# Kernel optimization log

Measured on AMD Instinct MI355X. Metric: run time of the kernel, lower is better.

Reference implementation:

```python
import jax, jax.numpy as jnp
import numpy as np

N = 10000   # nodes
E = 320000  # edges
G = 64      # graphs in batch
D = 256     # gnn embedding dim
A = 118     # atomic_num_dim
OUT = 100   # spectrum dim
NUM_GINE = 2


def setup_inputs() -> dict:
    key = jax.random.key(0)
    ks = jax.random.split(key, 16)
    inp = {
        'atomic_num': jax.random.normal(ks[0], (N, A), dtype=jnp.float32),
        'length': jax.random.uniform(ks[1], (E,), dtype=jnp.float32),
        'src': jax.random.randint(ks[2], (E,), 0, N, dtype=jnp.int32),
        'dst': jax.random.randint(ks[3], (E,), 0, N, dtype=jnp.int32),
        'graph_ids': jnp.sort(jax.random.randint(ks[4], (N,), 0, G, dtype=jnp.int32)),
        # parameters
        'W_node': jax.random.normal(ks[5], (A, D), dtype=jnp.float32) / np.sqrt(A),
        'b_node': jnp.zeros((D,), dtype=jnp.float32),
        'W_edge': jax.random.normal(ks[6], (1, D), dtype=jnp.float32),
        'b_edge': jnp.zeros((D,), dtype=jnp.float32),
        'gine_eps': jnp.zeros((NUM_GINE,), dtype=jnp.float32),  # learnable eps per GINEConv
        'W_gnn': jax.random.normal(ks[7], (NUM_GINE, D, D), dtype=jnp.float32) / np.sqrt(D),
        'b_gnn': jnp.zeros((NUM_GINE, D), dtype=jnp.float32),
        'eps_param': jnp.array([1e-3], dtype=jnp.float32),  # unify_vector eps
        'W_mlp': jax.random.normal(ks[8], (D, OUT), dtype=jnp.float32) / np.sqrt(D),
        'b_mlp': jnp.zeros((OUT,), dtype=jnp.float32),
    }
    return inp


def reference(atomic_num, length, src, dst, graph_ids,
              W_node, b_node, W_edge, b_edge,
              gine_eps, W_gnn, b_gnn, eps_param, W_mlp, b_mlp):
    # node / edge embeddings
    h = atomic_num @ W_node + b_node            # [N, D]
    e = length[:, None] @ W_edge + b_edge       # [E, D]
    # GINEConv layers: m_ij = relu(h_src + e_ij); h_i' = W((1+eps)h_i + sum_j m_ij) + b
    for i in range(NUM_GINE):
        m = jax.nn.relu(h[src] + e)             # [E, D] gather + elementwise
        agg = jax.ops.segment_sum(m, dst, num_segments=N)  # scatter-sum to dst nodes
        h = ((1.0 + gine_eps[i]) * h + agg) @ W_gnn[i] + b_gnn[i]
    # sum_nodes pooling per graph
    feat = jax.ops.segment_sum(h, graph_ids, num_segments=G)  # [G, D]
    # unify_vector: global min/max normalization
    mn = jnp.min(feat)
    mx = jnp.max(feat)
    feat = (feat - mn) / (eps_param[0] + mx - mn)
    # MLP head (no hidden layers): Linear(D, 100)
    return feat @ W_mlp + b_mlp                 # [G, 100]
```

## Files before the change

### kernel.cpp

```cpp
#include <hip/hip_runtime.h>
#include <hip/hip_bf16.h>

#define N_NODES 10000
#define N_EDGES 320000
#define N_GRAPHS 64
#define DIM 256
#define ADIM 118
#define OUTD 100
#define CAP 192

typedef short bf8_t __attribute__((ext_vector_type(8)));
typedef float f4_t  __attribute__((ext_vector_type(4)));

__device__ __forceinline__ unsigned short f2bf(float f) {
    unsigned u = __float_as_uint(f);
    u += 0x7FFFu + ((u >> 16) & 1u);
    return (unsigned short)(u >> 16);
}
__device__ __forceinline__ float bf2f(unsigned short s) {
    return __uint_as_float(((unsigned)s) << 16);
}

__global__ __launch_bounds__(256) void convW_k(
    const float* __restrict__ Wn, const float* __restrict__ Wg,
    unsigned short* __restrict__ WnT, unsigned short* __restrict__ WgT,
    int* __restrict__ cursor, float* __restrict__ feat) {
    int i = blockIdx.x * 256 + threadIdx.x;
    if (i < 32768) {
        int c = i >> 7, k = i & 127;
        WnT[i] = (k < ADIM) ? f2bf(Wn[k * DIM + c]) : (unsigned short)0;
    } else {
        int j = i - 32768;
        int l = j >> 16, rem = j & 65535;
        int c = rem >> 8, k = rem & 255;
        WgT[j] = f2bf(Wg[l * 65536 + k * DIM + c]);
    }
    if (i < N_NODES) cursor[i] = i * CAP;
    if (i < N_GRAPHS * DIM) feat[i] = 0.f;
}

__global__ __launch_bounds__(256) void fill_k(
    const int* __restrict__ src, const int* __restrict__ dst,
    const float* __restrict__ len, int* __restrict__ cursor,
    int2* __restrict__ epack) {
    int j = blockIdx.x * 256 + threadIdx.x;
    if (j >= N_EDGES) return;
    int d = dst[j];
    int pos = atomicAdd(&cursor[d], 1);
    if (pos < d * CAP + CAP)
        epack[pos] = make_int2(src[j], __float_as_int(len[j]));
}

#define AST 136
__global__ __launch_bounds__(256) void node_embed_k(
    const float* __restrict__ an, const unsigned short* __restrict__ WnT,
    const float* __restrict__ bn, unsigned short* __restrict__ hbf) {
    __shared__ unsigned short xs[16 * AST];
    const int base = blockIdx.x * 16;
    const int tid = threadIdx.x;
    for (int i = tid; i < 16 * (AST - ADIM); i += 256) {
        int r = i / (AST - ADIM);
        int c = i - r * (AST - ADIM);
        xs[r * AST + ADIM + c] = 0;
    }
    for (int i = tid; i < 16 * ADIM; i += 256) {
        int r = i / ADIM;
        int c = i - r * ADIM;
        xs[r * AST + c] = f2bf(an[(size_t)(base + r) * ADIM + c]);
    }
    __syncthreads();
    const int wave = tid >> 6, lane = tid & 63;
    const int m = lane & 15, quad = lane >> 4;
    bf8_t afrag[4];
    #pragma unroll
    for (int s = 0; s < 4; ++s)
        afrag[s] = *(const bf8_t*)&xs[m * AST + s * 32 + quad * 8];
    const int colbase = wave * 64;
    f4_t acc[4];
    #pragma unroll
    for (int ct = 0; ct < 4; ++ct) acc[ct] = (f4_t){0.f, 0.f, 0.f, 0.f};
    #pragma unroll
    for (int ct = 0; ct < 4; ++ct) {
        const unsigned short* wp = WnT + (size_t)(colbase + ct * 16 + m) * 128 + quad * 8;
        #pragma unroll
        for (int s = 0; s < 4; ++s) {
            bf8_t bfrag = *(const bf8_t*)(wp + s * 32);
            acc[ct] = __builtin_amdgcn_mfma_f32_16x16x32_bf16(afrag[s], bfrag, acc[ct], 0, 0, 0);
        }
    }
    #pragma unroll
    for (int ct = 0; ct < 4; ++ct) {
        int col = colbase + ct * 16 + m;
        float bb = bn[col];
        #pragma unroll
        for (int r = 0; r < 4; ++r)
            hbf[(size_t)(base + quad * 4 + r) * DIM + col] = f2bf(acc[ct][r] + bb);
    }
}

__global__ __launch_bounds__(256) void gather_k(
    const unsigned short* __restrict__ hbf, const int* __restrict__ cursor,
    const int2* __restrict__ epack, const float* __restrict__ We,
    const float* __restrict__ be, const float* __restrict__ epsp, int layer,
    unsigned short* __restrict__ xbf) {
    const int wave = threadIdx.x >> 6, lane = threadIdx.x & 63;
    const int node = __builtin_amdgcn_readfirstlane(blockIdx.x * 4 + wave);
    const int sub = lane >> 5;
    const int dp = (lane & 31) * 8;
    float4 wa = *(const float4*)(We + dp);
    float4 wc = *(const float4*)(We + dp + 4);
    float4 b0 = *(const float4*)(be + dp);
    float4 b1 = *(const float4*)(be + dp + 4);
    float w[8]  = {wa.x, wa.y, wa.z, wa.w, wc.x, wc.y, wc.z, wc.w};
    float bv[8] = {b0.x, b0.y, b0.z, b0.w, b1.x, b1.y, b1.z, b1.w};
    float acc[8];
    #pragma unroll
    for (int i = 0; i < 8; ++i) acc[i] = 0.f;
    const unsigned short* hb = hbf + dp;
    const int lo = node * CAP;
    const int cnt = min(__builtin_amdgcn_readfirstlane(cursor[node]) - lo, CAP);
    const int2* ep = epack + lo;
    int t = 0;
#define PAIR(pa, pb) { \
    int s = sub ? (pb).x : (pa).x; \
    float l = __int_as_float(sub ? (pb).y : (pa).y); \
    bf8_t a = *(const bf8_t*)(hb + (size_t)s * DIM); \
    _Pragma("unroll") \
    for (int d = 0; d < 8; ++d) \
        acc[d] += fmaxf(bf2f((unsigned short)a[d]) + fmaf(l, w[d], bv[d]), 0.f); }
    for (; t + 7 < cnt; t += 8) {
        int2 q0 = ep[t + 0], q1 = ep[t + 1], q2 = ep[t + 2], q3 = ep[t + 3];
        int2 q4 = ep[t + 4], q5 = ep[t + 5], q6 = ep[t + 6], q7 = ep[t + 7];
        PAIR(q0, q1) PAIR(q2, q3) PAIR(q4, q5) PAIR(q6, q7)
    }
    for (; t + 1 < cnt; t += 2) {
        int2 q0 = ep[t], q1 = ep[t + 1];
        PAIR(q0, q1)
    }
    if (t < cnt) {
        int2 q0 = ep[t];
        float l = __int_as_float(q0.y);
        bf8_t a = *(const bf8_t*)(hb + (size_t)q0.x * DIM);
        if (sub == 0) {
            #pragma unroll
            for (int d = 0; d < 8; ++d)
                acc[d] += fmaxf(bf2f((unsigned short)a[d]) + fmaf(l, w[d], bv[d]), 0.f);
        }
    }
#undef PAIR
    #pragma unroll
    for (int d = 0; d < 8; ++d)
        acc[d] += __shfl(acc[d], lane ^ 32, 64);
    if (sub == 0) {
        const float eps1 = 1.f + epsp[layer];
        bf8_t hv = *(const bf8_t*)(hbf + (size_t)node * DIM + dp);
        bf8_t o;
        #pragma unroll
        for (int d = 0; d < 8; ++d)
            o[d] = (short)f2bf(fmaf(eps1, bf2f((unsigned short)hv[d]), acc[d]));
        *(bf8_t*)(xbf + (size_t)node * DIM + dp) = o;
    }
}

#define XST 264
__global__ __launch_bounds__(256) void update_k(
    const unsigned short* __restrict__ xbf,
    const unsigned short* __restrict__ WT, const float* __restrict__ b,
    unsigned short* __restrict__ hout,
    const int* __restrict__ gid, float* __restrict__ feat, int do_pool) {
    __shared__ unsigned short xs[16 * XST];
    __shared__ int gids[16];
    const int rb = blockIdx.x >> 1;
    const int halfc = blockIdx.x & 1;
    const int base = rb * 16;
    const int tid = threadIdx.x;
    #pragma unroll
    for (int cch = tid; cch < 512; cch += 256) {
        int rr = cch >> 5, k0 = (cch & 31) * 8;
        *(bf8_t*)&xs[rr * XST + k0] = *(const bf8_t*)(xbf + (size_t)(base + rr) * DIM + k0);
    }
    if (do_pool && tid < 16) gids[tid] = gid[base + tid];
    __syncthreads();
    const int wave = tid >> 6, lane = tid & 63;
    const int m = lane & 15, quad = lane >> 4;
    bf8_t afrag[8];
    #pragma unroll
    for (int s = 0; s < 8; ++s)
        afrag[s] = *(const bf8_t*)&xs[m * XST + s * 32 + quad * 8];
    const int colbase = halfc * 128 + wave * 32;
    f4_t acc[2];
    #pragma unroll
    for (int ct = 0; ct < 2; ++ct) acc[ct] = (f4_t){0.f, 0.f, 0.f, 0.f};
    #pragma unroll
    for (int ct = 0; ct < 2; ++ct) {
        const unsigned short* wp = WT + (size_t)(colbase + ct * 16 + m) * DIM + quad * 8;
        #pragma unroll
        for (int s = 0; s < 8; ++s) {
            bf8_t bfrag = *(const bf8_t*)(wp + s * 32);
            acc[ct] = __builtin_amdgcn_mfma_f32_16x16x32_bf16(afrag[s], bfrag, acc[ct], 0, 0, 0);
        }
    }
    if (!do_pool) {
        #pragma unroll
        for (int ct = 0; ct < 2; ++ct) {
            int col = colbase + ct * 16 + m;
            float bb = b[col];
            #pragma unroll
            for (int r = 0; r < 4; ++r)
                hout[(size_t)(base + quad * 4 + r) * DIM + col] = f2bf(acc[ct][r] + bb);
        }
    } else {
        #pragma unroll
        for (int ct = 0; ct < 2; ++ct) {
            int col = colbase + ct * 16 + m;
            float bb = b[col];
            float run = 0.f;
            int cur = gids[quad * 4];
            #pragma unroll
            for (int r = 0; r < 4; ++r) {
                int g = gids[quad * 4 + r];
                if (g != cur) {
                    atomicAdd(&feat[(size_t)cur * DIM + col], run);
                    run = 0.f;
                    cur = g;
                }
                run += acc[ct][r] + bb;
            }
            atomicAdd(&feat[(size_t)cur * DIM + col], run);
        }
    }
}

__global__ __launch_bounds__(256) void headmm_k(
    const float* __restrict__ feat, const float* __restrict__ Wm,
    const float* __restrict__ bm, const float* __restrict__ epsp,
    float* __restrict__ out) {
    __shared__ float frow[DIM];
    __shared__ float smn[4], smx[4], sMn, sMx;
    const int g = blockIdx.x;
    const int tid = threadIdx.x;
    float mn = 3.4e38f, mx = -3.4e38f;
    for (int i = tid; i < N_GRAPHS * DIM; i += 256) {
        float v = feat[i];
        mn = fminf(mn, v);
        mx = fmaxf(mx, v);
    }
    frow[tid] = feat[g * DIM + tid];
    #pragma unroll
    for (int off = 32; off > 0; off >>= 1) {
        mn = fminf(mn, __shfl_down(mn, off, 64));
        mx = fmaxf(mx, __shfl_down(mx, off, 64));
    }
    const int wave = tid >> 6, lane = tid & 63;
    if (lane == 0) { smn[wave] = mn; smx[wave] = mx; }
    __syncthreads();
    if (tid == 0) {
        sMn = fminf(fminf(smn[0], smn[1]), fminf(smn[2], smn[3]));
        sMx = fmaxf(fmaxf(smx[0], smx[1]), fmaxf(smx[2], smx[3]));
    }
    __syncthreads();
    if (tid < OUTD) {
        const float mnv = sMn;
        const float inv = 1.f / (epsp[0] + sMx - mnv);
        float acc = 0.f;
        for (int d = 0; d < DIM; ++d)
            acc += (frow[d] - mnv) * Wm[d * OUTD + tid];
        out[g * OUTD + tid] = acc * inv + bm[tid];
    }
}

extern "C" void kernel_launch(void* const* d_in, const int* in_sizes, int n_in,
                              void* d_out, int out_size, void* d_ws, size_t ws_size,
                              hipStream_t stream) {
    const float* atomic_num = (const float*)d_in[0];
    const float* length     = (const float*)d_in[1];
    const int*   src        = (const int*)d_in[2];
    const int*   dst        = (const int*)d_in[3];
    const int*   gid        = (const int*)d_in[4];
    const float* W_node     = (const float*)d_in[5];
    const float* b_node     = (const float*)d_in[6];
    const float* W_edge     = (const float*)d_in[7];
    const float* b_edge     = (const float*)d_in[8];
    const float* gine_eps   = (const float*)d_in[9];
    const float* W_gnn      = (const float*)d_in[10];
    const float* b_gnn      = (const float*)d_in[11];
    const float* eps_param  = (const float*)d_in[12];
    const float* W_mlp      = (const float*)d_in[13];
    const float* b_mlp      = (const float*)d_in[14];
    float* out = (float*)d_out;

    float* feat = (float*)d_ws;
    int* cursor = (int*)(feat + (size_t)N_GRAPHS * DIM);
    int2* epack = (int2*)(cursor + N_NODES + 4);
    unsigned short* hbf0 = (unsigned short*)(epack + (size_t)N_NODES * CAP);
    unsigned short* hbf1 = hbf0 + (size_t)N_NODES * DIM;
    unsigned short* xbf  = hbf1 + (size_t)N_NODES * DIM;
    unsigned short* WnT  = xbf + (size_t)N_NODES * DIM;
    unsigned short* WgT  = WnT + 256 * 128;

    convW_k<<<640, 256, 0, stream>>>(W_node, W_gnn, WnT, WgT, cursor, feat);
    fill_k<<<N_EDGES / 256, 256, 0, stream>>>(src, dst, length, cursor, epack);
    node_embed_k<<<N_NODES / 16, 256, 0, stream>>>(atomic_num, WnT, b_node, hbf0);

    gather_k<<<N_NODES / 4, 256, 0, stream>>>(
        hbf0, cursor, epack, W_edge, b_edge, gine_eps, 0, xbf);
    update_k<<<(N_NODES / 16) * 2, 256, 0, stream>>>(
        xbf, WgT, b_gnn, hbf1, gid, feat, 0);
    gather_k<<<N_NODES / 4, 256, 0, stream>>>(
        hbf1, cursor, epack, W_edge, b_edge, gine_eps, 1, xbf);
    update_k<<<(N_NODES / 16) * 2, 256, 0, stream>>>(
        xbf, WgT + 256 * 256, b_gnn + DIM, hbf0, gid, feat, 1);

    headmm_k<<<N_GRAPHS, 256, 0, stream>>>(feat, W_mlp, b_mlp, eps_param, out);
}
```

Measured before the change: 217.8 us.

## Split gather across feature quarters with one scalar element per lane

Restructures the edge gather so that each wave covers one node and a 64-wide quarter of the feature dimension, with each lane loading a single bf16 element, instead of half-waves loading 8-element vectors across two edges. The grid grows fourfold and block indices are remapped so the four quarter-blocks of the same node group sit next to each other, which is meant to improve parallelism and keep loads coalesced. The output is written with a nontemporal store. In exchange, each edge index is now read four times and the row gathers become 2-byte scalar loads rather than 16-byte vector loads, which adds instruction and request overhead.

After: 228.5 us. 1.05x slower.

```diff
diff --git a/kernel.cpp b/kernel.cpp
--- a/kernel.cpp
+++ b/kernel.cpp
@@ -104,62 +104,49 @@
     const float* __restrict__ be, const float* __restrict__ epsp, int layer,
     unsigned short* __restrict__ xbf) {
     const int wave = threadIdx.x >> 6, lane = threadIdx.x & 63;
-    const int node = __builtin_amdgcn_readfirstlane(blockIdx.x * 4 + wave);
-    const int sub = lane >> 5;
-    const int dp = (lane & 31) * 8;
-    float4 wa = *(const float4*)(We + dp);
-    float4 wc = *(const float4*)(We + dp + 4);
-    float4 b0 = *(const float4*)(be + dp);
-    float4 b1 = *(const float4*)(be + dp + 4);
-    float w[8]  = {wa.x, wa.y, wa.z, wa.w, wc.x, wc.y, wc.z, wc.w};
-    float bv[8] = {b0.x, b0.y, b0.z, b0.w, b1.x, b1.y, b1.z, b1.w};
-    float acc[8];
-    #pragma unroll
-    for (int i = 0; i < 8; ++i) acc[i] = 0.f;
-    const unsigned short* hb = hbf + dp;
+    const int b = blockIdx.x;
+    const int quarter = b & 3;
+    const int node = __builtin_amdgcn_readfirstlane(
+        ((b >> 3) * 2 + ((b >> 2) & 1)) * 4 + wave);
+    const int d = quarter * 64 + lane;
+    const float w  = We[d];
+    const float bb = be[d];
+    const unsigned short* hb = hbf + d;
+    float acc = 0.f;
     const int lo = node * CAP;
     const int cnt = min(__builtin_amdgcn_readfirstlane(cursor[node]) - lo, CAP);
     const int2* ep = epack + lo;
     int t = 0;
-#define PAIR(pa, pb) { \
-    int s = sub ? (pb).x : (pa).x; \
-    float l = __int_as_float(sub ? (pb).y : (pa).y); \
-    bf8_t a = *(const bf8_t*)(hb + (size_t)s * DIM); \
-    _Pragma("unroll") \
-    for (int d = 0; d < 8; ++d) \
-        acc[d] += fmaxf(bf2f((unsigned short)a[d]) + fmaf(l, w[d], bv[d]), 0.f); }
     for (; t + 7 < cnt; t += 8) {
         int2 q0 = ep[t + 0], q1 = ep[t + 1], q2 = ep[t + 2], q3 = ep[t + 3];
         int2 q4 = ep[t + 4], q5 = ep[t + 5], q6 = ep[t + 6], q7 = ep[t + 7];
-        PAIR(q0, q1) PAIR(q2, q3) PAIR(q4, q5) PAIR(q6, q7)
-    }
-    for (; t + 1 < cnt; t += 2) {
-        int2 q0 = ep[t], q1 = ep[t + 1];
-        PAIR(q0, q1)
-    }
-    if (t < cnt) {
+        unsigned short a0 = hb[(size_t)q0.x * DIM];
+        unsigned short a1 = hb[(size_t)q1.x * DIM];
+        unsigned short a2 = hb[(size_t)q2.x * DIM];
+        unsigned short a3 = hb[(size_t)q3.x * DIM];
+        unsigned short a4 = hb[(size_t)q4.x * DIM];
+        unsigned short a5 = hb[(size_t)q5.x * DIM];
+        unsigned short a6 = hb[(size_t)q6.x * DIM];
+        unsigned short a7 = hb[(size_t)q7.x * DIM];
+        acc += fmaxf(bf2f(a0) + fmaf(__int_as_float(q0.y), w, bb), 0.f);
+        acc += fmaxf(bf2f(a1) + fmaf(__int_as_float(q1.y), w, bb), 0.f);
+        acc += fmaxf(bf2f(a2) + fmaf(__int_as_float(q2.y), w, bb), 0.f);
+        acc += fmaxf(bf2f(a3) + fmaf(__int_as_float(q3.y), w, bb), 0.f);
+        acc += fmaxf(bf2f(a4) + fmaf(__int_as_float(q4.y), w, bb), 0.f);
+        acc += fmaxf(bf2f(a5) + fmaf(__int_as_float(q5.y), w, bb), 0.f);
+        acc += fmaxf(bf2f(a6) + fmaf(__int_as_float(q6.y), w, bb), 0.f);
+        acc += fmaxf(bf2f(a7) + fmaf(__int_as_float(q7.y), w, bb), 0.f);
+    }
+    for (; t < cnt; ++t) {
         int2 q0 = ep[t];
-        float l = __int_as_float(q0.y);
-        bf8_t a = *(const bf8_t*)(hb + (size_t)q0.x * DIM);
-        if (sub == 0) {
-            #pragma unroll
-            for (int d = 0; d < 8; ++d)
-                acc[d] += fmaxf(bf2f((unsigned short)a[d]) + fmaf(l, w[d], bv[d]), 0.f);
-        }
-    }
-#undef PAIR
-    #pragma unroll
-    for (int d = 0; d < 8; ++d)
-        acc[d] += __shfl(acc[d], lane ^ 32, 64);
-    if (sub == 0) {
-        const float eps1 = 1.f + epsp[layer];
-        bf8_t hv = *(const bf8_t*)(hbf + (size_t)node * DIM + dp);
-        bf8_t o;
-        #pragma unroll
-        for (int d = 0; d < 8; ++d)
-            o[d] = (short)f2bf(fmaf(eps1, bf2f((unsigned short)hv[d]), acc[d]));
-        *(bf8_t*)(xbf + (size_t)node * DIM + dp) = o;
-    }
+        unsigned short a0 = hb[(size_t)q0.x * DIM];
+        acc += fmaxf(bf2f(a0) + fmaf(__int_as_float(q0.y), w, bb), 0.f);
+    }
+    const float eps1 = 1.f + epsp[layer];
+    float hv = bf2f(hb[(size_t)node * DIM]);
+    __builtin_nontemporal_store(
+        f2bf(fmaf(eps1, hv, acc)),
+        xbf + (size_t)node * DIM + d);
 }
 
 #define XST 264
@@ -302,11 +289,11 @@
     fill_k<<<N_EDGES / 256, 256, 0, stream>>>(src, dst, length, cursor, epack);
     node_embed_k<<<N_NODES / 16, 256, 0, stream>>>(atomic_num, WnT, b_node, hbf0);
 
-    gather_k<<<N_NODES / 4, 256, 0, stream>>>(
+    gather_k<<<N_NODES, 256, 0, stream>>>(
         hbf0, cursor, epack, W_edge, b_edge, gine_eps, 0, xbf);
     update_k<<<(N_NODES / 16) * 2, 256, 0, stream>>>(
         xbf, WgT, b_gnn, hbf1, gid, feat, 0);
-    gather_k<<<N_NODES / 4, 256, 0, stream>>>(
+    gather_k<<<N_NODES, 256, 0, stream>>>(
         hbf1, cursor, epack, W_edge, b_edge, gine_eps, 1, xbf);
     update_k<<<(N_NODES / 16) * 2, 256, 0, stream>>>(
         xbf, WgT + 256 * 256, b_gnn + DIM, hbf0, gid, feat, 1);
```

## Split edge gather into two passes by source-node half for cache locality

Applied to the files above, without the earlier changes.

Edges are bucketed by whether the source node falls in the first or second half of the node range, each half with its own 96-slot region per destination. Each GINE layer now runs the gather twice, once per half, so each pass touches only half of the bf16 node feature table, aiming to keep it resident in L2/MALL. The first pass writes fp32 partial sums to a new buffer that the second pass reads and combines with the self term. This adds an extra launch and a 10 MB fp32 round trip per layer. Per-destination capacity per half drops to 96, which risks dropping edges if in-degree from one half exceeds that.

After: 228.3 us. 1.05x slower.

```diff
diff --git a/kernel.cpp b/kernel.cpp
--- a/kernel.cpp
+++ b/kernel.cpp
@@ -35,7 +35,10 @@
         int c = rem >> 8, k = rem & 255;
         WgT[j] = f2bf(Wg[l * 65536 + k * DIM + c]);
     }
-    if (i < N_NODES) cursor[i] = i * CAP;
+    if (i < N_NODES) {
+        cursor[i] = i * CAP;
+        cursor[N_NODES + i] = i * CAP + 96;
+    }
     if (i < N_GRAPHS * DIM) feat[i] = 0.f;
 }
 
@@ -46,9 +49,14 @@
     int j = blockIdx.x * 256 + threadIdx.x;
     if (j >= N_EDGES) return;
     int d = dst[j];
-    int pos = atomicAdd(&cursor[d], 1);
-    if (pos < d * CAP + CAP)
-        epack[pos] = make_int2(src[j], __float_as_int(len[j]));
+    int s = src[j];
+    if (s < N_NODES / 2) {
+        int pos = atomicAdd(&cursor[d], 1);
+        if (pos < d * CAP + 96) epack[pos] = make_int2(s, __float_as_int(len[j]));
+    } else {
+        int pos = atomicAdd(&cursor[N_NODES + d], 1);
+        if (pos < d * CAP + CAP) epack[pos] = make_int2(s, __float_as_int(len[j]));
+    }
 }
 
 #define AST 136
@@ -102,7 +110,7 @@
     const unsigned short* __restrict__ hbf, const int* __restrict__ cursor,
     const int2* __restrict__ epack, const float* __restrict__ We,
     const float* __restrict__ be, const float* __restrict__ epsp, int layer,
-    unsigned short* __restrict__ xbf) {
+    float* __restrict__ xacc, unsigned short* __restrict__ xbf, int pass) {
     const int wave = threadIdx.x >> 6, lane = threadIdx.x & 63;
     const int node = __builtin_amdgcn_readfirstlane(blockIdx.x * 4 + wave);
     const int sub = lane >> 5;
@@ -117,9 +125,10 @@
     #pragma unroll
     for (int i = 0; i < 8; ++i) acc[i] = 0.f;
     const unsigned short* hb = hbf + dp;
-    const int lo = node * CAP;
-    const int cnt = min(__builtin_amdgcn_readfirstlane(cursor[node]) - lo, CAP);
-    const int2* ep = epack + lo;
+    const int base = node * CAP + (pass ? 96 : 0);
+    const int cnt = min(
+        __builtin_amdgcn_readfirstlane(cursor[pass ? N_NODES + node : node]) - base, 96);
+    const int2* ep = epack + base;
     int t = 0;
 #define PAIR(pa, pb) { \
     int s = sub ? (pb).x : (pa).x; \
@@ -152,13 +161,24 @@
     for (int d = 0; d < 8; ++d)
         acc[d] += __shfl(acc[d], lane ^ 32, 64);
     if (sub == 0) {
-        const float eps1 = 1.f + epsp[layer];
-        bf8_t hv = *(const bf8_t*)(hbf + (size_t)node * DIM + dp);
-        bf8_t o;
-        #pragma unroll
-        for (int d = 0; d < 8; ++d)
-            o[d] = (short)f2bf(fmaf(eps1, bf2f((unsigned short)hv[d]), acc[d]));
-        *(bf8_t*)(xbf + (size_t)node * DIM + dp) = o;
+        float* xp = xacc + (size_t)node * DIM + dp;
+        if (pass == 0) {
+            f4_t o0 = {acc[0], acc[1], acc[2], acc[3]};
+            f4_t o1 = {acc[4], acc[5], acc[6], acc[7]};
+            __builtin_nontemporal_store(o0, (f4_t*)xp);
+            __builtin_nontemporal_store(o1, (f4_t*)(xp + 4));
+        } else {
+            f4_t p0 = __builtin_nontemporal_load((const f4_t*)xp);
+            f4_t p1 = __builtin_nontemporal_load((const f4_t*)(xp + 4));
+            float pv[8] = {p0[0], p0[1], p0[2], p0[3], p1[0], p1[1], p1[2], p1[3]};
+            const float eps1 = 1.f + epsp[layer];
+            bf8_t hv = *(const bf8_t*)(hbf + (size_t)node * DIM + dp);
+            bf8_t o;
+            #pragma unroll
+            for (int d = 0; d < 8; ++d)
+                o[d] = (short)f2bf(fmaf(eps1, bf2f((unsigned short)hv[d]), acc[d] + pv[d]));
+            *(bf8_t*)(xbf + (size_t)node * DIM + dp) = o;
+        }
     }
 }
 
@@ -291,23 +311,28 @@
 
     float* feat = (float*)d_ws;
     int* cursor = (int*)(feat + (size_t)N_GRAPHS * DIM);
-    int2* epack = (int2*)(cursor + N_NODES + 4);
+    int2* epack = (int2*)(cursor + 2 * N_NODES + 4);
     unsigned short* hbf0 = (unsigned short*)(epack + (size_t)N_NODES * CAP);
     unsigned short* hbf1 = hbf0 + (size_t)N_NODES * DIM;
     unsigned short* xbf  = hbf1 + (size_t)N_NODES * DIM;
     unsigned short* WnT  = xbf + (size_t)N_NODES * DIM;
     unsigned short* WgT  = WnT + 256 * 128;
+    float* xacc = (float*)(WgT + 2 * 256 * 256);
 
     convW_k<<<640, 256, 0, stream>>>(W_node, W_gnn, WnT, WgT, cursor, feat);
     fill_k<<<N_EDGES / 256, 256, 0, stream>>>(src, dst, length, cursor, epack);
     node_embed_k<<<N_NODES / 16, 256, 0, stream>>>(atomic_num, WnT, b_node, hbf0);
 
     gather_k<<<N_NODES / 4, 256, 0, stream>>>(
-        hbf0, cursor, epack, W_edge, b_edge, gine_eps, 0, xbf);
+        hbf0, cursor, epack, W_edge, b_edge, gine_eps, 0, xacc, xbf, 0);
+    gather_k<<<N_NODES / 4, 256, 0, stream>>>(
+        hbf0, cursor, epack, W_edge, b_edge, gine_eps, 0, xacc, xbf, 1);
     update_k<<<(N_NODES / 16) * 2, 256, 0, stream>>>(
         xbf, WgT, b_gnn, hbf1, gid, feat, 0);
     gather_k<<<N_NODES / 4, 256, 0, stream>>>(
-        hbf1, cursor, epack, W_edge, b_edge, gine_eps, 1, xbf);
+        hbf1, cursor, epack, W_edge, b_edge, gine_eps, 1, xacc, xbf, 0);
+    gather_k<<<N_NODES / 4, 256, 0, stream>>>(
+        hbf1, cursor, epack, W_edge, b_edge, gine_eps, 1, xacc, xbf, 1);
     update_k<<<(N_NODES / 16) * 2, 256, 0, stream>>>(
         xbf, WgT + 256 * 256, b_gnn + DIM, hbf0, gid, feat, 1);
 
```
